# Kernel tuning notes

Hardware: AMD Instinct MI355X
Metric: run time of the kernel (lower is better)

Reference implementation:

```python
import jax, jax.numpy as jnp
import numpy as np

BASE_ALPHA = 0.05
NUM_ITER = 2
EPS = 1e-06


def setup_inputs() -> dict:
    key = jax.random.key(0)
    k1, k2 = jax.random.split(key)
    pred = jax.random.normal(k1, (8, 8192, 3), dtype=jnp.float32)
    partial = jax.random.normal(k2, (8, 2048, 3), dtype=jnp.float32)
    return {"pred": pred, "partial": partial}


def _cdist(a, b):
    # Euclidean pairwise distances via ||a||^2 - 2ab + ||b||^2 (avoids [B,N,M,3] temp).
    a2 = jnp.sum(a * a, axis=-1)  # [B,N]
    b2 = jnp.sum(b * b, axis=-1)  # [B,M]
    d2 = a2[:, :, None] - 2.0 * jnp.einsum('bnd,bmd->bnm', a, b) + b2[:, None, :]
    return jnp.sqrt(jnp.maximum(d2, 0.0))


def reference(pred, partial):
    refined = pred
    for _ in range(NUM_ITER):
        dist = _cdist(refined, partial)          # [B,N,M]
        min_dist = jnp.min(dist, axis=-1)        # [B,N]
        min_idx = jnp.argmin(dist, axis=-1)      # [B,N]
        nearest = jnp.take_along_axis(partial, min_idx[:, :, None], axis=1)  # [B,N,3]
        dist_norm = min_dist / (jnp.max(min_dist, axis=-1, keepdims=True) + EPS)
        alpha = BASE_ALPHA * (2.0 - dist_norm)   # [B,N]
        refined = refined + alpha[:, :, None] * (nearest - refined)
    return refined
```

## Files before the change

### kernel.cpp

```cpp
#include <hip/hip_runtime.h>
#include <math.h>

#define BATCH 8
#define NPRED 8192
#define MPART 2048
#define NPTS  (BATCH * NPRED)
#define MTOT  (BATCH * MPART)
#define QPL   4
#define QPB   256
#define WAVES 8
#define GPW   32
#define NNBLK (2 * NPTS / QPB)
#define NCMB  (NPTS / 1024)
#define BASE_ALPHA 0.05f
#define EPS 1e-6f

__global__ __launch_bounds__(256) void prep_kernel(const float* __restrict__ partial,
                                                   float* __restrict__ ppgf,
                                                   float4* __restrict__ near4) {
    const int m = blockIdx.x * 256 + threadIdx.x;
    const float* p = partial + 3u * (unsigned)m;
    const float x = p[0], y = p[1], z = p[2];
    const int g = m >> 2, c = m & 3;
    float* base = ppgf + (size_t)g * 16 + c;
    base[0]  = -2.0f * x;
    base[4]  = -2.0f * y;
    base[8]  = -2.0f * z;
    base[12] = fmaf(x, x, fmaf(y, y, z * z));
    near4[m] = make_float4(x, y, z, 0.0f);
}

template <bool FUSE>
__global__ __launch_bounds__(512, 4) void nn_kernel(
    const float* __restrict__ src,
    const float4* __restrict__ ppg,
    const float4* __restrict__ near4,
    const float* __restrict__ md_in,
    const int*   __restrict__ idx_in,
    const float* __restrict__ bmax_in,
    float* __restrict__ ref_out,
    unsigned long long* __restrict__ keys_out)
{
    __shared__ float4 tile[1024];
    unsigned long long* lk = (unsigned long long*)tile;

    const int qb   = blockIdx.x >> 1;
    const int half = blockIdx.x & 1;
    const int b    = qb >> 5;
    const int tid  = threadIdx.x;
    const int wave = tid >> 6, lane = tid & 63;

    const float4* gsrc = ppg + ((b << 11) + (half << 10));
    tile[tid]       = gsrc[tid];
    tile[tid + 512] = gsrc[tid + 512];

    float axq[QPL], ayq[QPL], azq[QPL], a2q[QPL];
    if (FUSE) {
        float v = bmax_in[(b << 3) + (lane & 7)];
        #pragma unroll
        for (int o = 32; o > 0; o >>= 1) v = fmaxf(v, __shfl_down(v, o, 64));
        const float maxv = __shfl(v, 0, 64);
        #pragma unroll
        for (int j = 0; j < QPL; ++j) {
            const int t = (qb << 8) + (j << 6) + lane;
            const float md = md_in[t];
            const int   id = idx_in[t];
            const float alpha = BASE_ALPHA * (2.0f - md / (maxv + EPS));
            const float4 nb = near4[(b << 11) + id];
            const float* p = src + 3u * (unsigned)t;
            const float px = p[0], py = p[1], pz = p[2];
            axq[j] = fmaf(alpha, nb.x - px, px);
            ayq[j] = fmaf(alpha, nb.y - py, py);
            azq[j] = fmaf(alpha, nb.z - pz, pz);
            if (half == 0 && wave == 0) {
                float* o = ref_out + 3u * (unsigned)t;
                o[0] = axq[j]; o[1] = ayq[j]; o[2] = azq[j];
            }
        }
    } else {
        #pragma unroll
        for (int j = 0; j < QPL; ++j) {
            const int t = (qb << 8) + (j << 6) + lane;
            const float* p = src + 3u * (unsigned)t;
            axq[j] = p[0]; ayq[j] = p[1]; azq[j] = p[2];
        }
    }
    #pragma unroll
    for (int j = 0; j < QPL; ++j)
        a2q[j] = fmaf(axq[j], axq[j], fmaf(ayq[j], ayq[j], azq[j] * azq[j]));

    __syncthreads();

    const float4* wp = tile + (wave << 7);
    float best[QPL]; int bg[QPL];
    #pragma unroll
    for (int j = 0; j < QPL; ++j) { best[j] = 1e30f; bg[j] = 0; }

    #pragma unroll 4
    for (int i = 0; i < GPW; ++i) {
        const float4 X = wp[4 * i + 0];
        const float4 Y = wp[4 * i + 1];
        const float4 Z = wp[4 * i + 2];
        const float4 W = wp[4 * i + 3];
        #pragma unroll
        for (int j = 0; j < QPL; ++j) {
            const float ax = axq[j], ay = ayq[j], az = azq[j];
            const float d0 = fmaf(Z.x, az, fmaf(Y.x, ay, fmaf(X.x, ax, W.x)));
            const float d1 = fmaf(Z.y, az, fmaf(Y.y, ay, fmaf(X.y, ax, W.y)));
            const float d2 = fmaf(Z.z, az, fmaf(Y.z, ay, fmaf(X.z, ax, W.z)));
            const float d3 = fmaf(Z.w, az, fmaf(Y.w, ay, fmaf(X.w, ax, W.w)));
            const float gm = fminf(fminf(d0, d1), fminf(d2, d3));
            if (gm < best[j]) bg[j] = i;
            best[j] = fminf(best[j], gm);
        }
    }

    unsigned long long key[QPL];
    #pragma unroll
    for (int j = 0; j < QPL; ++j) {
        const int gi = bg[j];
        const float4 X = wp[4 * gi + 0];
        const float4 Y = wp[4 * gi + 1];
        const float4 Z = wp[4 * gi + 2];
        const float4 W = wp[4 * gi + 3];
        const float ax = axq[j], ay = ayq[j], az = azq[j];
        const float d0 = fmaf(Z.x, az, fmaf(Y.x, ay, fmaf(X.x, ax, W.x)));
        const float d1 = fmaf(Z.y, az, fmaf(Y.y, ay, fmaf(X.y, ax, W.y)));
        const float d2 = fmaf(Z.z, az, fmaf(Y.z, ay, fmaf(X.z, ax, W.z)));
        const float bv = best[j];
        int c;
        if      (d0 == bv) c = 0;
        else if (d1 == bv) c = 1;
        else if (d2 == bv) c = 2;
        else               c = 3;
        const int m = (half << 10) + (wave << 7) + (gi << 2) + c;
        const float dd = fmaxf(bv + a2q[j], 0.0f);
        key[j] = ((unsigned long long)__float_as_uint(dd) << 32) | (unsigned)m;
    }

    __syncthreads();
    #pragma unroll
    for (int j = 0; j < QPL; ++j)
        lk[wave * QPB + (j << 6) + lane] = key[j];
    __syncthreads();

    if (wave < 4) {
        const int q2 = (wave << 6) + lane;
        unsigned long long kk = lk[q2];
        #pragma unroll
        for (int s = 1; s < WAVES; ++s) {
            const unsigned long long k = lk[s * QPB + q2];
            if (k < kk) kk = k;
        }
        keys_out[half * NPTS + (qb << 8) + q2] = kk;
    }
}

__global__ __launch_bounds__(1024) void combine_kernel(
    const unsigned long long* __restrict__ keys,
    float* __restrict__ md_out, int* __restrict__ idx_out,
    float* __restrict__ bmax_out)
{
    __shared__ float smax[16];
    const int t = blockIdx.x * 1024 + threadIdx.x;
    const int wave = threadIdx.x >> 6, lane = threadIdx.x & 63;
    const unsigned long long k0 = keys[t], k1 = keys[NPTS + t];
    const unsigned long long kk = (k1 < k0) ? k1 : k0;
    const float md = sqrtf(__uint_as_float((unsigned)(kk >> 32)));
    md_out[t]  = md;
    idx_out[t] = (int)(kk & 0xffffffffu);
    float w = md;
    #pragma unroll
    for (int o = 32; o > 0; o >>= 1) w = fmaxf(w, __shfl_down(w, o, 64));
    if (lane == 0) smax[wave] = w;
    __syncthreads();
    if (threadIdx.x < 64) {
        float v = smax[lane & 15];
        #pragma unroll
        for (int o = 32; o > 0; o >>= 1) v = fmaxf(v, __shfl_down(v, o, 64));
        if (lane == 0) bmax_out[blockIdx.x] = v;
    }
}

__global__ __launch_bounds__(256) void update_kernel(
    const float* __restrict__ ref1,
    const float4* __restrict__ near4,
    const float* __restrict__ md2,
    const int*   __restrict__ idx2,
    const float* __restrict__ bmax2,
    float* __restrict__ out)
{
    const int t = blockIdx.x * 256 + threadIdx.x;
    const int b = t >> 13;
    const int lane = threadIdx.x & 63;
    float v = bmax2[(b << 3) + (lane & 7)];
    #pragma unroll
    for (int o = 32; o > 0; o >>= 1) v = fmaxf(v, __shfl_down(v, o, 64));
    const float maxv = __shfl(v, 0, 64);
    const float md = md2[t];
    const int   id = idx2[t];
    const float alpha = BASE_ALPHA * (2.0f - md / (maxv + EPS));
    const float4 nb = near4[(b << 11) + id];
    const float* p = ref1 + 3u * (unsigned)t;
    const float px = p[0], py = p[1], pz = p[2];
    float* o = out + 3u * (unsigned)t;
    o[0] = fmaf(alpha, nb.x - px, px);
    o[1] = fmaf(alpha, nb.y - py, py);
    o[2] = fmaf(alpha, nb.z - pz, pz);
}

extern "C" void kernel_launch(void* const* d_in, const int* in_sizes, int n_in,
                              void* d_out, int out_size, void* d_ws, size_t ws_size,
                              hipStream_t stream) {
    const float* pred    = (const float*)d_in[0];
    const float* partial = (const float*)d_in[1];
    float* out = (float*)d_out;

    char* ws = (char*)d_ws;
    float4* ppg   = (float4*)ws;
    float4* near4 = (float4*)(ws + 262144);
    float*  ref1  = (float*)(ws + 524288);
    float*  md1   = (float*)(ws + 1310720);
    int*    idx1  = (int*)(ws + 1572864);
    unsigned long long* keys = (unsigned long long*)(ws + 1835008);
    float*  bmax1 = (float*)(ws + 2883584);
    float*  bmax2 = bmax1 + NCMB;

    prep_kernel<<<MTOT / 256, 256, 0, stream>>>(partial, (float*)ppg, near4);

    nn_kernel<false><<<NNBLK, 512, 0, stream>>>(
        pred, ppg, near4, nullptr, nullptr, nullptr, nullptr, keys);
    combine_kernel<<<NCMB, 1024, 0, stream>>>(keys, md1, idx1, bmax1);

    nn_kernel<true><<<NNBLK, 512, 0, stream>>>(
        pred, ppg, near4, md1, idx1, bmax1, ref1, keys);
    combine_kernel<<<NCMB, 1024, 0, stream>>>(keys, md1, idx1, bmax2);

    update_kernel<<<NPTS / 256, 256, 0, stream>>>(ref1, near4, md1, idx1, bmax2, out);
}
```

Before: 100.7 us.

## Split partial cloud into quarters with eight queries per lane

The NN kernel now splits each batch's partial points into four quarters instead of two. Each block stages 512 candidates in shared memory, and each lane handles 8 query points instead of 4, so every shared-memory load of a candidate group is reused across twice as many queries. The grid has the same number of blocks overall. The combine kernel now merges four partial keys per point, and the keys buffer and workspace offsets are enlarged to match. The trade-off is more registers per lane, which may lower occupancy, and twice the key traffic between the NN and combine kernels.

```diff
diff --git a/kernel.cpp b/kernel.cpp
--- a/kernel.cpp
+++ b/kernel.cpp
@@ -6,11 +6,13 @@
 #define MPART 2048
 #define NPTS  (BATCH * NPRED)
 #define MTOT  (BATCH * MPART)
-#define QPL   4
-#define QPB   256
+#define QPL   8
+#define QPB   512
 #define WAVES 8
-#define GPW   32
-#define NNBLK (2 * NPTS / QPB)
+#define QUARTERS 4
+#define PTS_PER_Q 512
+#define GPW   16
+#define NNBLK (QUARTERS * NPTS / QPB)
 #define NCMB  (NPTS / 1024)
 #define BASE_ALPHA 0.05f
 #define EPS 1e-6f
@@ -41,20 +43,18 @@
     float* __restrict__ ref_out,
     unsigned long long* __restrict__ keys_out)
 {
-    __shared__ float4 tile[1024];
-    unsigned long long* lk = (unsigned long long*)tile;
-
-    const int qb   = blockIdx.x >> 1;
-    const int half = blockIdx.x & 1;
-    const int b    = qb >> 5;
-    const int tid  = threadIdx.x;
-    const int wave = tid >> 6, lane = tid & 63;
-
-    const float4* gsrc = ppg + ((b << 11) + (half << 10));
-    tile[tid]       = gsrc[tid];
-    tile[tid + 512] = gsrc[tid + 512];
-
-    float axq[QPL], ayq[QPL], azq[QPL], a2q[QPL];
+    __shared__ __align__(16) unsigned long long lk[WAVES * QPB];
+    float4* tile = (float4*)lk;
+
+    const int qb      = blockIdx.x >> 2;
+    const int quarter = blockIdx.x & 3;
+    const int b       = qb >> 4;
+    const int tid     = threadIdx.x;
+    const int wave    = tid >> 6, lane = tid & 63;
+
+    tile[tid] = ppg[(b << 11) + (quarter << 9) + tid];
+
+    float axq[QPL], ayq[QPL], azq[QPL];
     if (FUSE) {
         float v = bmax_in[(b << 3) + (lane & 7)];
         #pragma unroll
@@ -62,7 +62,7 @@
         const float maxv = __shfl(v, 0, 64);
         #pragma unroll
         for (int j = 0; j < QPL; ++j) {
-            const int t = (qb << 8) + (j << 6) + lane;
+            const int t = (qb << 9) + (j << 6) + lane;
             const float md = md_in[t];
             const int   id = idx_in[t];
             const float alpha = BASE_ALPHA * (2.0f - md / (maxv + EPS));
@@ -72,7 +72,7 @@
             axq[j] = fmaf(alpha, nb.x - px, px);
             ayq[j] = fmaf(alpha, nb.y - py, py);
             azq[j] = fmaf(alpha, nb.z - pz, pz);
-            if (half == 0 && wave == 0) {
+            if (quarter == 0 && wave == 0) {
                 float* o = ref_out + 3u * (unsigned)t;
                 o[0] = axq[j]; o[1] = ayq[j]; o[2] = azq[j];
             }
@@ -80,23 +80,20 @@
     } else {
         #pragma unroll
         for (int j = 0; j < QPL; ++j) {
-            const int t = (qb << 8) + (j << 6) + lane;
+            const int t = (qb << 9) + (j << 6) + lane;
             const float* p = src + 3u * (unsigned)t;
             axq[j] = p[0]; ayq[j] = p[1]; azq[j] = p[2];
         }
     }
-    #pragma unroll
-    for (int j = 0; j < QPL; ++j)
-        a2q[j] = fmaf(axq[j], axq[j], fmaf(ayq[j], ayq[j], azq[j] * azq[j]));
-
-    __syncthreads();
-
-    const float4* wp = tile + (wave << 7);
+
+    __syncthreads();
+
+    const float4* wp = tile + (wave << 6);
     float best[QPL]; int bg[QPL];
     #pragma unroll
     for (int j = 0; j < QPL; ++j) { best[j] = 1e30f; bg[j] = 0; }
 
-    #pragma unroll 4
+    #pragma unroll 2
     for (int i = 0; i < GPW; ++i) {
         const float4 X = wp[4 * i + 0];
         const float4 Y = wp[4 * i + 1];
@@ -133,8 +130,9 @@
         else if (d1 == bv) c = 1;
         else if (d2 == bv) c = 2;
         else               c = 3;
-        const int m = (half << 10) + (wave << 7) + (gi << 2) + c;
-        const float dd = fmaxf(bv + a2q[j], 0.0f);
+        const int m = (quarter << 9) + (wave << 6) + (gi << 2) + c;
+        const float a2 = fmaf(ax, ax, fmaf(ay, ay, az * az));
+        const float dd = fmaxf(bv + a2, 0.0f);
         key[j] = ((unsigned long long)__float_as_uint(dd) << 32) | (unsigned)m;
     }
 
@@ -144,16 +142,13 @@
         lk[wave * QPB + (j << 6) + lane] = key[j];
     __syncthreads();
 
-    if (wave < 4) {
-        const int q2 = (wave << 6) + lane;
-        unsigned long long kk = lk[q2];
-        #pragma unroll
-        for (int s = 1; s < WAVES; ++s) {
-            const unsigned long long k = lk[s * QPB + q2];
-            if (k < kk) kk = k;
-        }
-        keys_out[half * NPTS + (qb << 8) + q2] = kk;
-    }
+    unsigned long long kk = lk[tid];
+    #pragma unroll
+    for (int s = 1; s < WAVES; ++s) {
+        const unsigned long long k = lk[s * QPB + tid];
+        if (k < kk) kk = k;
+    }
+    keys_out[quarter * NPTS + (qb << 9) + tid] = kk;
 }
 
 __global__ __launch_bounds__(1024) void combine_kernel(
@@ -164,8 +159,14 @@
     __shared__ float smax[16];
     const int t = blockIdx.x * 1024 + threadIdx.x;
     const int wave = threadIdx.x >> 6, lane = threadIdx.x & 63;
-    const unsigned long long k0 = keys[t], k1 = keys[NPTS + t];
-    const unsigned long long kk = (k1 < k0) ? k1 : k0;
+    const unsigned long long k0 = keys[t];
+    const unsigned long long k1 = keys[NPTS + t];
+    const unsigned long long k2 = keys[2 * NPTS + t];
+    const unsigned long long k3 = keys[3 * NPTS + t];
+    unsigned long long kk = k0;
+    if (k1 < kk) kk = k1;
+    if (k2 < kk) kk = k2;
+    if (k3 < kk) kk = k3;
     const float md = sqrtf(__uint_as_float((unsigned)(kk >> 32)));
     md_out[t]  = md;
     idx_out[t] = (int)(kk & 0xffffffffu);
@@ -223,7 +224,7 @@
     float*  md1   = (float*)(ws + 1310720);
     int*    idx1  = (int*)(ws + 1572864);
     unsigned long long* keys = (unsigned long long*)(ws + 1835008);
-    float*  bmax1 = (float*)(ws + 2883584);
+    float*  bmax1 = (float*)(ws + 3932160);
     float*  bmax2 = bmax1 + NCMB;
 
     prep_kernel<<<MTOT / 256, 256, 0, stream>>>(partial, (float*)ppg, near4);
```

New measurement: 104.5 us. 1.04x slower.
